# Optimization experiments

Measured on AMD Instinct MI355X. Metric: run time of the kernel, lower is better.

Reference implementation:

```python
import math
import jax, jax.numpy as jnp
import numpy as np

D_MODEL = 1024
N_HEADS = 16
D_K = D_MODEL // N_HEADS
LQ, LK, B = 2048, 2048, 2


def setup_inputs() -> dict:
    key = jax.random.key(0)
    ks = jax.random.split(key, 12)
    q = jax.random.normal(ks[0], (LQ, B, D_MODEL), dtype=jnp.float32)
    k = jax.random.normal(ks[1], (LK, B, D_MODEL), dtype=jnp.float32)
    v = jax.random.normal(ks[2], (LK, B, D_MODEL), dtype=jnp.float32)
    # causal mask: scores with mask==0 are filled with -1e9
    mask = jnp.tril(jnp.ones((LQ, LK), dtype=jnp.int32))
    s = 0.02
    w_q = jax.random.normal(ks[3], (D_MODEL, D_MODEL), jnp.float32) * s
    b_q = jnp.zeros((D_MODEL,), jnp.float32)
    w_k = jax.random.normal(ks[4], (D_MODEL, D_MODEL), jnp.float32) * s
    b_k = jnp.zeros((D_MODEL,), jnp.float32)
    w_v = jax.random.normal(ks[5], (D_MODEL, D_MODEL), jnp.float32) * s
    b_v = jnp.zeros((D_MODEL,), jnp.float32)
    w_o = jax.random.normal(ks[6], (D_MODEL, D_MODEL), jnp.float32) * s
    b_o = jnp.zeros((D_MODEL,), jnp.float32)
    return {"query": q, "key": k, "value": v, "mask": mask,
            "w_q": w_q, "b_q": b_q, "w_k": w_k, "b_k": b_k,
            "w_v": w_v, "b_v": b_v, "w_o": w_o, "b_o": b_o}


def reference(query, key, value, mask, w_q, b_q, w_k, b_k, w_v, b_v, w_o, b_o):
    # dropout layers are identity (eval mode)
    Lq, Bsz, D = query.shape
    Lk = key.shape[0]
    scale = math.sqrt(D_K)
    # seq-first linear projections, then [L,B,D] -> [B,H,L,dk]
    def proj(x, w, b, L):
        y = x @ w.T + b
        return y.reshape(L, Bsz, N_HEADS, D_K).transpose(1, 2, 0, 3)
    Q = proj(query, w_q, b_q, Lq)   # [B,H,Lq,dk]
    K = proj(key, w_k, b_k, Lk)     # [B,H,Lk,dk]
    V = proj(value, w_v, b_v, Lk)   # [B,H,Lk,dk]
    scores = jnp.einsum('bhqd,bhkd->bhqk', Q, K) / scale
    m = mask[None, None, :, :]  # 2D mask broadcast path of original
    scores = jnp.where(m == 0, jnp.float32(-1e9), scores)
    attn = jax.nn.softmax(scores, axis=-1)  # [B,H,Lq,Lk]
    out = jnp.einsum('bhqk,bhkd->bhqd', attn, V)  # [B,H,Lq,dk]
    # replicate torch: transpose(0,1) -> [H,B,Lq,dk], flat view to [Lq,B,D]
    out = jnp.transpose(out, (1, 0, 2, 3)).reshape(Lq, Bsz, D)
    output = out @ w_o.T + b_o
    return output, attn
```

## Files before the change

kernel.cpp:

```cpp
#include <hip/hip_runtime.h>
#include <cstdint>

#define DM    1024
#define NH    16
#define DKH   64
#define SEQ   2048
#define BSZ   2
#define MROWS 4096

typedef __attribute__((ext_vector_type(8))) short bf16x8;
typedef __attribute__((ext_vector_type(4))) float f32x4;

__device__ __forceinline__ f32x4 mfma16(bf16x8 a, bf16x8 b, f32x4 c){
  return __builtin_amdgcn_mfma_f32_16x16x32_bf16(a, b, c, 0, 0, 0);
}

__device__ __forceinline__ ushort f2bf(float f){
  unsigned u = __float_as_uint(f);
  return (ushort)((u + 0x7FFFu + ((u >> 16) & 1u)) >> 16);
}

__device__ __forceinline__ void gload16(const ushort* g, ushort* l){
  __builtin_amdgcn_global_load_lds(
      (const __attribute__((address_space(1))) void*)g,
      (__attribute__((address_space(3))) void*)l, 16, 0, 0);
}

__device__ __forceinline__ void ntstore4(float* p, f32x4 v){
  __builtin_nontemporal_store(v, (f32x4*)p);
}

__global__ void cast_all(const float* __restrict__ q, const float* __restrict__ k,
                         const float* __restrict__ v, const float* __restrict__ wq,
                         const float* __restrict__ wk, const float* __restrict__ wv,
                         const float* __restrict__ wo,
                         ushort* __restrict__ qb, ushort* __restrict__ kb,
                         ushort* __restrict__ vb, ushort* __restrict__ wqb,
                         ushort* __restrict__ wkb, ushort* __restrict__ wvb,
                         ushort* __restrict__ wob)
{
  const int NB = (MROWS*DM)/4;
  const int NW = (DM*DM)/4;
  int stride = gridDim.x*blockDim.x;
  for (int i = blockIdx.x*blockDim.x + threadIdx.x; i < 3*NB; i += stride){
    int sel = i >> 20, j = i & (NB-1);
    const float4 x = ((const float4*)(sel==0?q:sel==1?k:v))[j];
    ushort4 o; o.x=f2bf(x.x); o.y=f2bf(x.y); o.z=f2bf(x.z); o.w=f2bf(x.w);
    ((ushort4*)(sel==0?qb:sel==1?kb:vb))[j] = o;
  }
  for (int i = blockIdx.x*blockDim.x + threadIdx.x; i < 4*NW; i += stride){
    int sel = i >> 18, j = i & (NW-1);
    const float4 x = ((const float4*)(sel==0?wq:sel==1?wk:sel==2?wv:wo))[j];
    ushort4 o; o.x=f2bf(x.x); o.y=f2bf(x.y); o.z=f2bf(x.z); o.w=f2bf(x.w);
    ((ushort4*)(sel==0?wqb:sel==1?wkb:sel==2?wvb:wob))[j] = o;
  }
}

__device__ __forceinline__ void gemm_body128(const ushort* __restrict__ A,
                                             const ushort* __restrict__ W,
                                             const float* __restrict__ bias,
                                             ushort* __restrict__ outp)
{
  __shared__ ushort As[128*32];
  __shared__ ushort Bs[128*32];
  const int tid = threadIdx.x, w = tid>>6, l = tid&63;
  const int wr = w>>1, wc = w&1, lr = l&15, lg = l>>4;
  const int bm = blockIdx.x, bn = blockIdx.y;
  const ushort* Ab = A + (size_t)bm*128*DM;
  const ushort* Wb = W + (size_t)bn*128*DM;
  f32x4 z4 = {0.f,0.f,0.f,0.f};
  f32x4 acc[4][4];
  #pragma unroll
  for (int i=0;i<4;i++){ acc[i][0]=z4; acc[i][1]=z4; acc[i][2]=z4; acc[i][3]=z4; }

  for (int k0 = 0; k0 < DM; k0 += 32){
    __syncthreads();
    #pragma unroll
    for (int i=0;i<2;i++){
      int idx = w*2+i;
      int row = idx*16 + (l>>2);
      int cg  = (l&3)*8;
      gload16(&Ab[(size_t)row*DM + k0 + cg], &As[idx*512]);
      gload16(&Wb[(size_t)row*DM + k0 + cg], &Bs[idx*512]);
    }
    __syncthreads();
    bf16x8 af[4], bw[4];
    #pragma unroll
    for (int t=0;t<4;t++) af[t] = *(const bf16x8*)&As[(wr*64 + t*16 + lr)*32 + lg*8];
    #pragma unroll
    for (int t=0;t<4;t++) bw[t] = *(const bf16x8*)&Bs[(wc*64 + t*16 + lr)*32 + lg*8];
    #pragma unroll
    for (int tm=0;tm<4;tm++)
      #pragma unroll
      for (int tn=0;tn<4;tn++)
        acc[tm][tn] = mfma16(af[tm], bw[tn], acc[tm][tn]);
  }
  #pragma unroll
  for (int tn=0;tn<4;tn++){
    int col = bn*128 + wc*64 + tn*16 + lr;
    float bv = bias[col];
    #pragma unroll
    for (int tm=0;tm<4;tm++){
      #pragma unroll
      for (int r=0;r<4;r++){
        int row = bm*128 + wr*64 + tm*16 + lg*4 + r;
        outp[(size_t)row*DM + col] = f2bf(acc[tm][tn][r] + bv);
      }
    }
  }
}

__global__ __launch_bounds__(256) void gemm_qkv(
    const ushort* __restrict__ A0, const ushort* __restrict__ A1, const ushort* __restrict__ A2,
    const ushort* __restrict__ W0, const ushort* __restrict__ W1, const ushort* __restrict__ W2,
    const float* __restrict__ b0, const float* __restrict__ b1, const float* __restrict__ b2,
    ushort* __restrict__ O0, ushort* __restrict__ O1, ushort* __restrict__ O2)
{
  int z = blockIdx.z;
  const ushort* A = (z==0)?A0:((z==1)?A1:A2);
  const ushort* W = (z==0)?W0:((z==1)?W1:W2);
  const float*  b = (z==0)?b0:((z==1)?b1:b2);
  ushort*       O = (z==0)?O0:((z==1)?O1:O2);
  gemm_body128(A, W, b, O);
}

__global__ __launch_bounds__(256) void gemm_fin64(const ushort* __restrict__ A,
                                                  const ushort* __restrict__ W,
                                                  const float* __restrict__ bias,
                                                  float* __restrict__ O)
{
  __shared__ ushort As[64*32];
  __shared__ ushort Bs[128*32];
  const int tid = threadIdx.x, w = tid>>6, l = tid&63;
  const int wr = w>>1, wc = w&1, lr = l&15, lg = l>>4;
  const int bm = blockIdx.x, bn = blockIdx.y;
  const ushort* Ab = A + (size_t)bm*64*DM;
  const ushort* Wb = W + (size_t)bn*128*DM;
  f32x4 z4 = {0.f,0.f,0.f,0.f};
  f32x4 acc[2][4];
  #pragma unroll
  for (int i=0;i<2;i++){ acc[i][0]=z4; acc[i][1]=z4; acc[i][2]=z4; acc[i][3]=z4; }

  for (int k0 = 0; k0 < DM; k0 += 32){
    __syncthreads();
    {
      int row = w*16 + (l>>2);
      int cg  = (l&3)*8;
      gload16(&Ab[(size_t)row*DM + k0 + cg], &As[w*512]);
    }
    #pragma unroll
    for (int i=0;i<2;i++){
      int idx = w*2+i;
      int row = idx*16 + (l>>2);
      int cg  = (l&3)*8;
      gload16(&Wb[(size_t)row*DM + k0 + cg], &Bs[idx*512]);
    }
    __syncthreads();
    bf16x8 af[2], bw[4];
    #pragma unroll
    for (int t=0;t<2;t++) af[t] = *(const bf16x8*)&As[(wr*32 + t*16 + lr)*32 + lg*8];
    #pragma unroll
    for (int t=0;t<4;t++) bw[t] = *(const bf16x8*)&Bs[(wc*64 + t*16 + lr)*32 + lg*8];
    #pragma unroll
    for (int tm=0;tm<2;tm++)
      #pragma unroll
      for (int tn=0;tn<4;tn++)
        acc[tm][tn] = mfma16(af[tm], bw[tn], acc[tm][tn]);
  }
  #pragma unroll
  for (int tn=0;tn<4;tn++){
    int col = bn*128 + wc*64 + tn*16 + lr;
    float bv = bias[col];
    #pragma unroll
    for (int tm=0;tm<2;tm++){
      #pragma unroll
      for (int r=0;r<4;r++){
        int row = bm*64 + wr*32 + tm*16 + lg*4 + r;
        O[(size_t)row*DM + col] = acc[tm][tn][r] + bv;
      }
    }
  }
}

__global__ __launch_bounds__(256) void transpose_v(const ushort* __restrict__ Vp,
                                                   ushort* __restrict__ Vt)
{
  __shared__ ushort Ts[64*72];
  const int lt = blockIdx.x;
  const int h  = blockIdx.y;
  const int b  = blockIdx.z;
  const int tid = threadIdx.x;
  const int sr = tid>>3, sc = (tid&7)*8;
  uint4 v0 = *(const uint4*)&Vp[((size_t)(lt*64+sr)*BSZ + b)*DM + h*DKH + sc];
  uint4 v1 = *(const uint4*)&Vp[((size_t)(lt*64+sr+32)*BSZ + b)*DM + h*DKH + sc];
  const ushort* p0 = (const ushort*)&v0;
  const ushort* p1 = (const ushort*)&v1;
  #pragma unroll
  for (int j=0;j<8;j++){
    Ts[(sc+j)*72 + sr]    = p0[j];
    Ts[(sc+j)*72 + sr+32] = p1[j];
  }
  __syncthreads();
  const size_t ob = (size_t)((b*NH+h)*DKH);
  *(uint4*)&Vt[(ob + sr)*SEQ + lt*64 + sc]    = *(const uint4*)&Ts[sr*72 + sc];
  *(uint4*)&Vt[(ob + sr+32)*SEQ + lt*64 + sc] = *(const uint4*)&Ts[(sr+32)*72 + sc];
}

__global__ __launch_bounds__(256, 5) void attn_fused(const ushort* __restrict__ Qp,
                                                     const ushort* __restrict__ Kp,
                                                     const ushort* __restrict__ Vt,
                                                     float* __restrict__ attn,
                                                     ushort* __restrict__ ctx)
{
  __shared__ ushort Ks[64*72];
  __shared__ ushort Vs[64*72];
  __shared__ ushort Ps[4][16*72];
  const int bid0 = blockIdx.x;
  const int xcd = bid0 & 7, slot = bid0 >> 3;
  const int grp = xcd + 8*(slot & 3);
  const int ds  = slot >> 2;
  const int qt  = (ds & 1) ? (ds >> 1) : (31 - (ds >> 1));
  const int h = grp & 15, b = grp >> 4;
  const int q0 = qt*64;
  const int rounds = qt + 1;
  const int tid = threadIdx.x, w = tid>>6, l = tid&63;
  const int lr = l&15, lg = l>>4;
  ushort* Pw = &Ps[w][0];
  const size_t attnBase = (size_t)(b*NH+h)*SEQ*SEQ;
  const int qrow = q0 + w*16;
  const int sr = tid>>3, sc = (tid&7)*8;
  const ushort* Kg = Kp + (size_t)b*DM + h*DKH;
  const ushort* Vg = Vt + (size_t)((b*NH+h)*DKH)*SEQ;

  bf16x8 aq0 = *(const bf16x8*)&Qp[((size_t)(qrow+lr)*BSZ + b)*DM + h*DKH + lg*8];
  bf16x8 aq1 = *(const bf16x8*)&Qp[((size_t)(qrow+lr)*BSZ + b)*DM + h*DKH + 32 + lg*8];

  float rs[4] = {0.f,0.f,0.f,0.f};
  uint4 ka0 = *(const uint4*)&Kg[(size_t)(sr)*BSZ*DM + sc];
  uint4 ka1 = *(const uint4*)&Kg[(size_t)(sr+32)*BSZ*DM + sc];
  for (int r = 0; r < rounds; r++){
    __syncthreads();
    *(uint4*)&Ks[sr*72+sc]      = ka0;
    *(uint4*)&Ks[(sr+32)*72+sc] = ka1;
    if (r+1 < rounds){
      ka0 = *(const uint4*)&Kg[(size_t)((r+1)*64+sr)*BSZ*DM + sc];
      ka1 = *(const uint4*)&Kg[(size_t)((r+1)*64+sr+32)*BSZ*DM + sc];
    }
    __syncthreads();
    #pragma unroll
    for (int nt=0; nt<4; nt++){
      f32x4 s4 = {0.f,0.f,0.f,0.f};
      bf16x8 bk0 = *(const bf16x8*)&Ks[(nt*16+lr)*72 + lg*8];
      bf16x8 bk1 = *(const bf16x8*)&Ks[(nt*16+lr)*72 + 32 + lg*8];
      s4 = mfma16(aq0, bk0, s4);
      s4 = mfma16(aq1, bk1, s4);
      int kc = r*64 + nt*16 + lr;
      #pragma unroll
      for (int r4=0;r4<4;r4++){
        int qr = qrow + lg*4 + r4;
        float e = exp2f(s4[r4]*0.18033688011112042f);
        rs[r4] += (kc <= qr) ? e : 0.f;
      }
    }
  }
  float rinv[4];
  #pragma unroll
  for (int r4=0;r4<4;r4++){
    float vs = rs[r4];
    vs += __shfl_xor(vs, 1, 16);
    vs += __shfl_xor(vs, 2, 16);
    vs += __shfl_xor(vs, 4, 16);
    vs += __shfl_xor(vs, 8, 16);
    rinv[r4] = 1.0f / vs;
  }

  f32x4 z4 = {0.f,0.f,0.f,0.f};
  f32x4 oacc[4] = {z4,z4,z4,z4};
  uint4 kb0 = *(const uint4*)&Kg[(size_t)(sr)*BSZ*DM + sc];
  uint4 kb1 = *(const uint4*)&Kg[(size_t)(sr+32)*BSZ*DM + sc];
  uint4 vb0 = *(const uint4*)&Vg[(size_t)(sr)*SEQ + sc];
  uint4 vb1 = *(const uint4*)&Vg[(size_t)(sr+32)*SEQ + sc];
  for (int r = 0; r < rounds; r++){
    __syncthreads();
    *(uint4*)&Ks[sr*72+sc]      = kb0;
    *(uint4*)&Ks[(sr+32)*72+sc] = kb1;
    *(uint4*)&Vs[sr*72+sc]      = vb0;
    *(uint4*)&Vs[(sr+32)*72+sc] = vb1;
    if (r+1 < rounds){
      kb0 = *(const uint4*)&Kg[(size_t)((r+1)*64+sr)*BSZ*DM + sc];
      kb1 = *(const uint4*)&Kg[(size_t)((r+1)*64+sr+32)*BSZ*DM + sc];
      vb0 = *(const uint4*)&Vg[(size_t)(sr)*SEQ + (r+1)*64 + sc];
      vb1 = *(const uint4*)&Vg[(size_t)(sr+32)*SEQ + (r+1)*64 + sc];
    }
    __syncthreads();
    const int k0 = r*64;
    #pragma unroll
    for (int nt=0; nt<4; nt++){
      f32x4 s4 = {0.f,0.f,0.f,0.f};
      bf16x8 bk0 = *(const bf16x8*)&Ks[(nt*16+lr)*72 + lg*8];
      bf16x8 bk1 = *(const bf16x8*)&Ks[(nt*16+lr)*72 + 32 + lg*8];
      s4 = mfma16(aq0, bk0, s4);
      s4 = mfma16(aq1, bk1, s4);
      int kc = k0 + nt*16 + lr;
      #pragma unroll
      for (int r4=0;r4<4;r4++){
        int qg = qrow + lg*4 + r4;
        float p = (kc <= qg) ? exp2f(s4[r4]*0.18033688011112042f)*rinv[r4] : 0.f;
        Pw[(lg*4+r4)*72 + nt*16 + lr] = f2bf(p);
      }
    }
    #pragma unroll
    for (int pass=0; pass<4; pass++){
      int row16 = pass*4 + lg;
      ushort4 pv = *(const ushort4*)&Pw[row16*72 + lr*4];
      f32x4 o;
      o.x = __uint_as_float(((unsigned)pv.x) << 16);
      o.y = __uint_as_float(((unsigned)pv.y) << 16);
      o.z = __uint_as_float(((unsigned)pv.z) << 16);
      o.w = __uint_as_float(((unsigned)pv.w) << 16);
      ntstore4(&attn[attnBase + (size_t)(qrow + row16)*SEQ + k0 + lr*4], o);
    }
    bf16x8 pa0 = *(const bf16x8*)&Pw[lr*72 + lg*8];
    bf16x8 pa1 = *(const bf16x8*)&Pw[lr*72 + 32 + lg*8];
    #pragma unroll
    for (int nt=0; nt<4; nt++){
      bf16x8 vv0 = *(const bf16x8*)&Vs[(nt*16+lr)*72 + lg*8];
      bf16x8 vv1 = *(const bf16x8*)&Vs[(nt*16+lr)*72 + 32 + lg*8];
      oacc[nt] = mfma16(pa0, vv0, oacc[nt]);
      oacc[nt] = mfma16(pa1, vv1, oacc[nt]);
    }
  }
  #pragma unroll
  for (int nt=0;nt<4;nt++){
    #pragma unroll
    for (int r4=0;r4<4;r4++){
      int qg = qrow + lg*4 + r4;
      ctx[((size_t)(h*BSZ+b)*SEQ + qg)*DKH + nt*16 + lr] = f2bf(oacc[nt][r4]);
    }
  }
  int z0 = rounds*64;
  if (z0 < SEQ){
    f32x4 zz = {0.f,0.f,0.f,0.f};
    for (int r16=0; r16<16; r16++){
      float* rowp = attn + attnBase + (size_t)(qrow + r16)*SEQ;
      for (int c = z0 + l*4; c < SEQ; c += 256)
        ntstore4(&rowp[c], zz);
    }
  }
}

extern "C" void kernel_launch(void* const* d_in, const int* in_sizes, int n_in,
                              void* d_out, int out_size, void* d_ws, size_t ws_size,
                              hipStream_t stream)
{
  (void)in_sizes; (void)n_in; (void)out_size; (void)ws_size;
  const float* q  = (const float*)d_in[0];
  const float* k  = (const float*)d_in[1];
  const float* v  = (const float*)d_in[2];
  const float* wq = (const float*)d_in[4];
  const float* bq = (const float*)d_in[5];
  const float* wk = (const float*)d_in[6];
  const float* bk = (const float*)d_in[7];
  const float* wv = (const float*)d_in[8];
  const float* bv = (const float*)d_in[9];
  const float* wo = (const float*)d_in[10];
  const float* bo = (const float*)d_in[11];

  char* ws = (char*)d_ws;
  const size_t SZ_BIG = (size_t)MROWS*DM*2;
  const size_t SZ_W   = (size_t)DM*DM*2;
  ushort* Qb  = (ushort*)(ws);
  ushort* Kb  = (ushort*)(ws + SZ_BIG);
  ushort* Vb  = (ushort*)(ws + 2*SZ_BIG);
  ushort* Wqb = (ushort*)(ws + 3*SZ_BIG);
  ushort* Wkb = (ushort*)(ws + 3*SZ_BIG + SZ_W);
  ushort* Wvb = (ushort*)(ws + 3*SZ_BIG + 2*SZ_W);
  ushort* Wob = (ushort*)(ws + 3*SZ_BIG + 3*SZ_W);
  ushort* Qp  = (ushort*)(ws + 3*SZ_BIG + 4*SZ_W);
  ushort* Kp  = (ushort*)(ws + 4*SZ_BIG + 4*SZ_W);
  ushort* Vp  = (ushort*)(ws + 5*SZ_BIG + 4*SZ_W);
  ushort* Ctx = (ushort*)(ws + 6*SZ_BIG + 4*SZ_W);
  ushort* Vt  = Qb;

  float* out  = (float*)d_out;
  float* attn = out + (size_t)SEQ*BSZ*DM;

  cast_all<<<2048, 256, 0, stream>>>(q,k,v,wq,wk,wv,wo, Qb,Kb,Vb,Wqb,Wkb,Wvb,Wob);
  dim3 gq(32, 8, 3);
  gemm_qkv<<<gq, 256, 0, stream>>>(Qb,Kb,Vb, Wqb,Wkb,Wvb, bq,bk,bv, Qp,Kp,Vp);
  dim3 gt(32, NH, BSZ);
  transpose_v<<<gt, 256, 0, stream>>>(Vp, Vt);
  attn_fused<<<1024, 256, 0, stream>>>(Qp, Kp, Vt, attn, Ctx);
  dim3 gf(64, 8, 1);
  gemm_fin64<<<gf, 256, 0, stream>>>(Ctx, Wob, bo, out);
}
```

Measured before the change: 217.1 us.

## Move causal zero-fill of attention matrix into the cast/prep kernel

The writes of zeros to the upper-triangular (masked) part of the attention output move out of the fused attention kernel and into the first kernel, which now runs extra blocks that do the zero-fill alongside the fp32-to-bf16 casts. This takes heavy store traffic out of the imbalanced attention kernel's tail and overlaps it with the bandwidth-bound cast work. It assumes the attention kernel never writes those masked regions, so the block mapping in both kernels must agree.

```diff
diff --git a/kernel.cpp b/kernel.cpp
--- a/kernel.cpp
+++ b/kernel.cpp
@@ -30,25 +30,42 @@
   __builtin_nontemporal_store(v, (f32x4*)p);
 }
 
-__global__ void cast_all(const float* __restrict__ q, const float* __restrict__ k,
-                         const float* __restrict__ v, const float* __restrict__ wq,
-                         const float* __restrict__ wk, const float* __restrict__ wv,
-                         const float* __restrict__ wo,
-                         ushort* __restrict__ qb, ushort* __restrict__ kb,
-                         ushort* __restrict__ vb, ushort* __restrict__ wqb,
-                         ushort* __restrict__ wkb, ushort* __restrict__ wvb,
-                         ushort* __restrict__ wob)
-{
+__global__ void prep(const float* __restrict__ q, const float* __restrict__ k,
+                     const float* __restrict__ v, const float* __restrict__ wq,
+                     const float* __restrict__ wk, const float* __restrict__ wv,
+                     const float* __restrict__ wo,
+                     ushort* __restrict__ qb, ushort* __restrict__ kb,
+                     ushort* __restrict__ vb, ushort* __restrict__ wqb,
+                     ushort* __restrict__ wkb, ushort* __restrict__ wvb,
+                     ushort* __restrict__ wob, float* __restrict__ attn)
+{
+  const int bid = blockIdx.x;
+  if (bid < 1024){
+    const int qt = bid & 31, grp = bid >> 5;
+    if (qt == 31) return;
+    const int w = threadIdx.x >> 6, l = threadIdx.x & 63;
+    const size_t base = (size_t)grp * SEQ * SEQ;
+    const int zc = (qt + 1) * 64;
+    const int W4 = (SEQ - zc) >> 2;
+    f32x4 zz = {0.f,0.f,0.f,0.f};
+    for (int rr = 0; rr < 16; rr++){
+      float* rowp = attn + base + (size_t)(qt*64 + w*16 + rr)*SEQ + zc;
+      for (int c = l; c < W4; c += 64)
+        ntstore4(rowp + c*4, zz);
+    }
+    return;
+  }
   const int NB = (MROWS*DM)/4;
   const int NW = (DM*DM)/4;
-  int stride = gridDim.x*blockDim.x;
-  for (int i = blockIdx.x*blockDim.x + threadIdx.x; i < 3*NB; i += stride){
+  const int stride = 2048*256;
+  const int start = (bid - 1024)*256 + threadIdx.x;
+  for (int i = start; i < 3*NB; i += stride){
     int sel = i >> 20, j = i & (NB-1);
     const float4 x = ((const float4*)(sel==0?q:sel==1?k:v))[j];
     ushort4 o; o.x=f2bf(x.x); o.y=f2bf(x.y); o.z=f2bf(x.z); o.w=f2bf(x.w);
     ((ushort4*)(sel==0?qb:sel==1?kb:vb))[j] = o;
   }
-  for (int i = blockIdx.x*blockDim.x + threadIdx.x; i < 4*NW; i += stride){
+  for (int i = start; i < 4*NW; i += stride){
     int sel = i >> 18, j = i & (NW-1);
     const float4 x = ((const float4*)(sel==0?wq:sel==1?wk:sel==2?wv:wo))[j];
     ushort4 o; o.x=f2bf(x.x); o.y=f2bf(x.y); o.z=f2bf(x.z); o.w=f2bf(x.w);
@@ -338,15 +355,6 @@
       ctx[((size_t)(h*BSZ+b)*SEQ + qg)*DKH + nt*16 + lr] = f2bf(oacc[nt][r4]);
     }
   }
-  int z0 = rounds*64;
-  if (z0 < SEQ){
-    f32x4 zz = {0.f,0.f,0.f,0.f};
-    for (int r16=0; r16<16; r16++){
-      float* rowp = attn + attnBase + (size_t)(qrow + r16)*SEQ;
-      for (int c = z0 + l*4; c < SEQ; c += 256)
-        ntstore4(&rowp[c], zz);
-    }
-  }
 }
 
 extern "C" void kernel_launch(void* const* d_in, const int* in_sizes, int n_in,
@@ -385,7 +393,7 @@
   float* out  = (float*)d_out;
   float* attn = out + (size_t)SEQ*BSZ*DM;
 
-  cast_all<<<2048, 256, 0, stream>>>(q,k,v,wq,wk,wv,wo, Qb,Kb,Vb,Wqb,Wkb,Wvb,Wob);
+  prep<<<3072, 256, 0, stream>>>(q,k,v,wq,wk,wv,wo, Qb,Kb,Vb,Wqb,Wkb,Wvb,Wob, attn);
   dim3 gq(32, 8, 3);
   gemm_qkv<<<gq, 256, 0, stream>>>(Qb,Kb,Vb, Wqb,Wkb,Wvb, bq,bk,bv, Qp,Kp,Vp);
   dim3 gt(32, NH, BSZ);
```

Result: slower. 242.4 us (+11.6%).

## Read K and V fragments directly from global memory instead of LDS staging

Applied to the files above, without the earlier changes.

Removes the shared-memory K/V tiles and the block-wide barriers that staged them, and instead has each wave load its MFMA B-operand fragments straight from global memory (relying on L1/L2 caching since four waves read the same tile). This drops the two __syncthreads per round and LDS traffic and shrinks the LDS footprint, so waves progress independently. In exchange, global/cache traffic per block rises roughly fourfold and the software prefetch of the next tile is lost, so load latency is exposed.

```diff
diff --git a/kernel.cpp b/kernel.cpp
--- a/kernel.cpp
+++ b/kernel.cpp
@@ -212,8 +212,6 @@
                                                      float* __restrict__ attn,
                                                      ushort* __restrict__ ctx)
 {
-  __shared__ ushort Ks[64*72];
-  __shared__ ushort Vs[64*72];
   __shared__ ushort Ps[4][16*72];
   const int bid0 = blockIdx.x;
   const int xcd = bid0 & 7, slot = bid0 >> 3;
@@ -228,31 +226,23 @@
   ushort* Pw = &Ps[w][0];
   const size_t attnBase = (size_t)(b*NH+h)*SEQ*SEQ;
   const int qrow = q0 + w*16;
-  const int sr = tid>>3, sc = (tid&7)*8;
   const ushort* Kg = Kp + (size_t)b*DM + h*DKH;
   const ushort* Vg = Vt + (size_t)((b*NH+h)*DKH)*SEQ;
+  const size_t KROW = (size_t)BSZ*DM;
 
   bf16x8 aq0 = *(const bf16x8*)&Qp[((size_t)(qrow+lr)*BSZ + b)*DM + h*DKH + lg*8];
   bf16x8 aq1 = *(const bf16x8*)&Qp[((size_t)(qrow+lr)*BSZ + b)*DM + h*DKH + 32 + lg*8];
+  f32x4 z4 = {0.f,0.f,0.f,0.f};
 
   float rs[4] = {0.f,0.f,0.f,0.f};
-  uint4 ka0 = *(const uint4*)&Kg[(size_t)(sr)*BSZ*DM + sc];
-  uint4 ka1 = *(const uint4*)&Kg[(size_t)(sr+32)*BSZ*DM + sc];
   for (int r = 0; r < rounds; r++){
-    __syncthreads();
-    *(uint4*)&Ks[sr*72+sc]      = ka0;
-    *(uint4*)&Ks[(sr+32)*72+sc] = ka1;
-    if (r+1 < rounds){
-      ka0 = *(const uint4*)&Kg[(size_t)((r+1)*64+sr)*BSZ*DM + sc];
-      ka1 = *(const uint4*)&Kg[(size_t)((r+1)*64+sr+32)*BSZ*DM + sc];
-    }
-    __syncthreads();
+    const ushort* kt = Kg + (size_t)r*64*KROW;
     #pragma unroll
     for (int nt=0; nt<4; nt++){
-      f32x4 s4 = {0.f,0.f,0.f,0.f};
-      bf16x8 bk0 = *(const bf16x8*)&Ks[(nt*16+lr)*72 + lg*8];
-      bf16x8 bk1 = *(const bf16x8*)&Ks[(nt*16+lr)*72 + 32 + lg*8];
-      s4 = mfma16(aq0, bk0, s4);
+      const ushort* kr = kt + (size_t)(nt*16+lr)*KROW;
+      bf16x8 bk0 = *(const bf16x8*)&kr[lg*8];
+      bf16x8 bk1 = *(const bf16x8*)&kr[32 + lg*8];
+      f32x4 s4 = mfma16(aq0, bk0, z4);
       s4 = mfma16(aq1, bk1, s4);
       int kc = r*64 + nt*16 + lr;
       #pragma unroll
@@ -274,32 +264,16 @@
     rinv[r4] = 1.0f / vs;
   }
 
-  f32x4 z4 = {0.f,0.f,0.f,0.f};
   f32x4 oacc[4] = {z4,z4,z4,z4};
-  uint4 kb0 = *(const uint4*)&Kg[(size_t)(sr)*BSZ*DM + sc];
-  uint4 kb1 = *(const uint4*)&Kg[(size_t)(sr+32)*BSZ*DM + sc];
-  uint4 vb0 = *(const uint4*)&Vg[(size_t)(sr)*SEQ + sc];
-  uint4 vb1 = *(const uint4*)&Vg[(size_t)(sr+32)*SEQ + sc];
   for (int r = 0; r < rounds; r++){
-    __syncthreads();
-    *(uint4*)&Ks[sr*72+sc]      = kb0;
-    *(uint4*)&Ks[(sr+32)*72+sc] = kb1;
-    *(uint4*)&Vs[sr*72+sc]      = vb0;
-    *(uint4*)&Vs[(sr+32)*72+sc] = vb1;
-    if (r+1 < rounds){
-      kb0 = *(const uint4*)&Kg[(size_t)((r+1)*64+sr)*BSZ*DM + sc];
-      kb1 = *(const uint4*)&Kg[(size_t)((r+1)*64+sr+32)*BSZ*DM + sc];
-      vb0 = *(const uint4*)&Vg[(size_t)(sr)*SEQ + (r+1)*64 + sc];
-      vb1 = *(const uint4*)&Vg[(size_t)(sr+32)*SEQ + (r+1)*64 + sc];
-    }
-    __syncthreads();
     const int k0 = r*64;
+    const ushort* kt = Kg + (size_t)k0*KROW;
     #pragma unroll
     for (int nt=0; nt<4; nt++){
-      f32x4 s4 = {0.f,0.f,0.f,0.f};
-      bf16x8 bk0 = *(const bf16x8*)&Ks[(nt*16+lr)*72 + lg*8];
-      bf16x8 bk1 = *(const bf16x8*)&Ks[(nt*16+lr)*72 + 32 + lg*8];
-      s4 = mfma16(aq0, bk0, s4);
+      const ushort* kr = kt + (size_t)(nt*16+lr)*KROW;
+      bf16x8 bk0 = *(const bf16x8*)&kr[lg*8];
+      bf16x8 bk1 = *(const bf16x8*)&kr[32 + lg*8];
+      f32x4 s4 = mfma16(aq0, bk0, z4);
       s4 = mfma16(aq1, bk1, s4);
       int kc = k0 + nt*16 + lr;
       #pragma unroll
@@ -324,8 +298,9 @@
     bf16x8 pa1 = *(const bf16x8*)&Pw[lr*72 + 32 + lg*8];
     #pragma unroll
     for (int nt=0; nt<4; nt++){
-      bf16x8 vv0 = *(const bf16x8*)&Vs[(nt*16+lr)*72 + lg*8];
-      bf16x8 vv1 = *(const bf16x8*)&Vs[(nt*16+lr)*72 + 32 + lg*8];
+      const ushort* vr = &Vg[(size_t)(nt*16+lr)*SEQ + k0];
+      bf16x8 vv0 = *(const bf16x8*)&vr[lg*8];
+      bf16x8 vv1 = *(const bf16x8*)&vr[32 + lg*8];
       oacc[nt] = mfma16(pa0, vv0, oacc[nt]);
       oacc[nt] = mfma16(pa1, vv1, oacc[nt]);
     }
```

Result: slower. 367.5 us (+69.3%).
